# Performance work log

Hardware: AMD Instinct MI355X
Metric: run time of the kernel (lower is better)

Reference implementation:

```python
import jax, jax.numpy as jnp
import numpy as np

N_ATOMS = 50_000
N_PAIRS = 1_000_000
F_A = 75    # n_atom_input_feat
F_P = 14    # n_pair_input_feat
H = 50      # all hidden / output widths


def _glorot(key, shape):
    fan_in, fan_out = shape
    lim = np.sqrt(6.0 / (fan_in + fan_out)).astype(np.float32)
    return jax.random.uniform(key, shape, jnp.float32, -lim, lim)


def setup_inputs() -> dict:
    key = jax.random.key(0)
    ks = jax.random.split(key, 12)
    atom_features = jax.random.normal(ks[0], (N_ATOMS, F_A), jnp.float32)
    pair_features = jax.random.normal(ks[1], (N_PAIRS, F_P), jnp.float32)
    # per-pair anchor-atom segment id (sorted, as pairs are grouped by atom)
    pair_seg = jnp.sort(jax.random.randint(ks[2], (N_PAIRS,), 0, N_ATOMS, jnp.int32))
    atom_to_pair = jax.random.randint(ks[3], (N_PAIRS, 2), 0, N_ATOMS, jnp.int32)
    return {
        "atom_features": atom_features,
        "pair_features": pair_features,
        "pair_seg": pair_seg,
        "atom_to_pair": atom_to_pair,
        "W_AA": _glorot(ks[4], (F_A, H)), "b_AA": jnp.zeros((H,), jnp.float32),
        "W_PA": _glorot(ks[5], (F_P, H)), "b_PA": jnp.zeros((H,), jnp.float32),
        "W_A": _glorot(ks[6], (2 * H, H)), "b_A": jnp.zeros((H,), jnp.float32),
        "W_AP": _glorot(ks[7], (2 * F_A, H)), "b_AP": jnp.zeros((H,), jnp.float32),
        "W_PP": _glorot(ks[8], (F_P, H)), "b_PP": jnp.zeros((H,), jnp.float32),
        "W_P": _glorot(ks[9], (2 * H, H)), "b_P": jnp.zeros((H,), jnp.float32),
    }


def reference(atom_features, pair_features, pair_seg, atom_to_pair,
              W_AA, b_AA, W_PA, b_PA, W_A, b_A, W_AP, b_AP, W_PP, b_PP, W_P, b_P):
    act = jax.nn.relu
    n_atoms = atom_features.shape[0]
    n_pairs = pair_features.shape[0]

    # atom -> atom
    AA = act(atom_features @ W_AA + b_AA)                              # [Na, H]
    # pair -> atom: per-pair hidden, segment-summed to the anchor atom
    PA = act(pair_features @ W_PA + b_PA)                              # [Np, H]
    PA_sum = jax.ops.segment_sum(PA, pair_seg, num_segments=n_atoms)   # [Na, H]
    A = act(jnp.concatenate([AA, PA_sum], axis=1) @ W_A + b_A)         # [Na, H]

    # atom -> pair: gather both endpoints, (i,j) and (j,i) orderings
    ap = atom_features[atom_to_pair]                                   # [Np, 2, Fa]
    AP_ij = act(ap.reshape(n_pairs, 2 * ap.shape[-1]) @ W_AP + b_AP)
    AP_ji = act(ap[:, ::-1, :].reshape(n_pairs, 2 * ap.shape[-1]) @ W_AP + b_AP)
    # pair -> pair
    PP = act(pair_features @ W_PP + b_PP)
    P = act(jnp.concatenate([AP_ij + AP_ji, PP], axis=1) @ W_P + b_P)  # [Np, H]
    return A, P
```

## Files before the change

kernel.cpp:

```cpp
#include <hip/hip_runtime.h>
#include <hip/hip_bf16.h>

#define NA 50000
#define NP 1000000
#define FA 75
#define FP 14
#define H  50

typedef __attribute__((ext_vector_type(8))) short short8;
typedef __attribute__((ext_vector_type(4))) float f32x4;
typedef __attribute__((ext_vector_type(2))) float f32x2;

__device__ __forceinline__ ushort f2bf(float f) {
    union { float f; unsigned u; } v; v.f = f;
    unsigned r = v.u + 0x7FFF + ((v.u >> 16) & 1);
    return (ushort)(r >> 16);
}
__device__ __forceinline__ unsigned cvtpk(float lo, float hi) {
    unsigned r;
    asm("v_cvt_pk_bf16_f32 %0, %1, %2" : "=v"(r) : "v"(lo), "v"(hi));
    return r;
}
__device__ __forceinline__ ushort f2bf1(float f) { return (ushort)cvtpk(f, f); }
__device__ __forceinline__ unsigned pk_fp8(float u, float v) {
    unsigned r;
    asm("v_cvt_pk_fp8_f32 %0, %1, %2" : "=v"(r) : "v"(u), "v"(v));
    return r;
}
__device__ __forceinline__ float2 unpk_fp8(unsigned w) {
    float2 r;
    asm("v_cvt_pk_f32_fp8 %0, %1" : "=v"(r) : "v"(w));
    return r;
}
__device__ __forceinline__ short8 mk8(unsigned a, unsigned b, unsigned c, unsigned d) {
    union { unsigned u[4]; short8 s; } x; x.u[0]=a; x.u[1]=b; x.u[2]=c; x.u[3]=d; return x.s;
}

__global__ __launch_bounds__(256) void k_prep_frags(
    const float* __restrict__ W_P, const float* __restrict__ W_A,
    const float* __restrict__ W_PP, const float* __restrict__ W_PA,
    const float* __restrict__ W_AA, const float* __restrict__ W_AP,
    ushort* __restrict__ WPf, ushort* __restrict__ WAf, ushort* __restrict__ W2f,
    ushort* __restrict__ WPREf)
{
    const int t0 = blockIdx.x * 256 + threadIdx.x;
    const int STR = 16 * 256;
    for (int idx = t0; idx < 4*4*64*8; idx += STR) {
        int j = idx & 7, l = (idx >> 3) & 63, tn = (idx >> 9) & 3, tk = idx >> 11;
        int k = tk*32 + (l>>4)*8 + j;
        int c = tn*16 + (l&15);
        ushort vp = 0, va = 0;
        if (k < 100 && c < 50) { vp = f2bf(W_P[k*50+c]); va = f2bf(W_A[k*50+c]); }
        WPf[idx] = vp; WAf[idx] = va;
    }
    for (int idx = t0; idx < 8*64*8; idx += STR) {
        int j = idx & 7, l = (idx >> 3) & 63, tn = idx >> 9;
        int k = (l>>4)*8 + j;
        int c = (tn&3)*16 + (l&15);
        ushort v = 0;
        if (k < 14 && c < 50) v = f2bf(tn < 4 ? W_PP[k*50+c] : W_PA[k*50+c]);
        W2f[idx] = v;
    }
    for (int idx = t0; idx < 3*12*64*8; idx += STR) {
        int j = idx & 7, l = (idx >> 3) & 63;
        int g = idx >> 9;
        int tn = g % 12, tk = g / 12;
        int k = tk*32 + (l>>4)*8 + j;
        int sn = tn*16 + (l&15);
        int which = sn >> 6, col = sn & 63;
        ushort v = 0;
        if (k < FA && col < H) {
            float w = (which == 0) ? W_AA[k*H+col]
                    : (which == 1) ? W_AP[k*H+col]
                                   : W_AP[(FA+k)*H+col];
            v = f2bf(w);
        }
        WPREf[idx] = v;
    }
}

__global__ __launch_bounds__(256) void k_atom_pre(
    const float* __restrict__ af, const ushort* __restrict__ WPREf,
    const float* __restrict__ b_AA,
    ushort* __restrict__ AAb, ushort* __restrict__ UV8)
{
    __shared__ __align__(16) ushort sAF[64][104];
    const int t = threadIdx.x, lane = t & 63, w = t >> 6;
    const int a0 = blockIdx.x * 64, row0 = w * 16;

    for (int idx = t; idx < 64*96; idx += 256) {
        int r = idx / 96, c = idx % 96;
        int ag = a0 + r;
        float v = (c < FA && ag < NA) ? __builtin_nontemporal_load(&af[(size_t)ag*FA + c]) : 0.f;
        sAF[r][c] = f2bf(v);
    }
    __syncthreads();

    short8 afr[3];
    #pragma unroll
    for (int tk = 0; tk < 3; ++tk)
        afr[tk] = *(const short8*)&sAF[row0 + (lane&15)][tk*32 + (lane>>4)*8];

    const short8* B = (const short8*)WPREf;
    f32x4 acc[12];
    #pragma unroll
    for (int tn = 0; tn < 12; ++tn) acc[tn] = (f32x4){0.f, 0.f, 0.f, 0.f};
    #pragma unroll
    for (int tk = 0; tk < 3; ++tk) {
        #pragma unroll
        for (int tn = 0; tn < 12; ++tn) {
            short8 b = B[(tk*12 + tn)*64 + lane];
            acc[tn] = __builtin_amdgcn_mfma_f32_16x16x32_bf16(afr[tk], b, acc[tn], 0, 0, 0);
        }
    }

    #pragma unroll
    for (int tn = 0; tn < 4; ++tn) {
        int col = tn*16 + (lane&15);
        if (col < H) {
            float ba = b_AA[col];
            #pragma unroll
            for (int reg = 0; reg < 4; ++reg) {
                int atom = a0 + row0 + (lane>>4)*4 + reg;
                if (atom < NA) {
                    AAb[(size_t)atom*H + col] = f2bf(fmaxf(acc[tn][reg] + ba, 0.f));
                    UV8[(size_t)atom*64 + col] =
                        (ushort)pk_fp8(acc[4 + tn][reg], acc[8 + tn][reg]);
                }
            }
        }
    }
}

__global__ __launch_bounds__(256, 4) void k_pairs(
    const float* __restrict__ pf, const int* __restrict__ seg, const int* __restrict__ a2p,
    const ushort* __restrict__ UV8,
    const float* __restrict__ b_PP, const float* __restrict__ b_PA,
    const float* __restrict__ b_AP, const float* __restrict__ b_P,
    const ushort* __restrict__ WPf, const ushort* __restrict__ W2f,
    float* __restrict__ PAsum, float* __restrict__ Pout)
{
    __shared__ __align__(16) ushort sX[64][136];

    const int t = threadIdx.x;
    const int w = t >> 6, lane = t & 63;
    const int q = lane >> 4, m = lane & 15;
    const int p0 = blockIdx.x * 64;
    const int row0 = w * 16;
    const int p0w_u = __builtin_amdgcn_readfirstlane(p0 + row0);

    const int* a2ps = a2p + 2 * p0w_u;
    const int* segs = seg + p0w_u;
    int pi[16], pj[16], sg[16];
    #pragma unroll
    for (int it = 0; it < 16; ++it) {
        pi[it] = a2ps[2*it];
        pj[it] = a2ps[2*it + 1];
        sg[it] = segs[it];
    }

    const f32x2* pf2 = (const f32x2*)(pf + (size_t)(p0w_u + m) * FP);
    f32x2 g0 = {0.f,0.f}, g1 = {0.f,0.f}, g2 = {0.f,0.f}, g3 = {0.f,0.f};
    if (q == 0) {
        g0 = __builtin_nontemporal_load(&pf2[0]);
        g1 = __builtin_nontemporal_load(&pf2[1]);
        g2 = __builtin_nontemporal_load(&pf2[2]);
        g3 = __builtin_nontemporal_load(&pf2[3]);
    } else if (q == 1) {
        g0 = __builtin_nontemporal_load(&pf2[4]);
        g1 = __builtin_nontemporal_load(&pf2[5]);
        g2 = __builtin_nontemporal_load(&pf2[6]);
    }
    float bap = (lane < H) ? b_AP[lane] : 0.f;
    __builtin_amdgcn_sched_barrier(0);

    unsigned uvi[16], uvj[16];
    const unsigned lo2 = (unsigned)(lane << 1);
    #pragma unroll
    for (int it = 0; it < 8; ++it) {
        unsigned offi = ((unsigned)pi[it] << 7) | lo2;
        unsigned offj = ((unsigned)pj[it] << 7) | lo2;
        asm volatile("global_load_ushort %0, %1, %2"
                     : "=v"(uvi[it]) : "v"(offi), "s"(UV8));
        asm volatile("global_load_ushort %0, %1, %2"
                     : "=v"(uvj[it]) : "v"(offj), "s"(UV8));
    }
    #pragma unroll
    for (int it = 8; it < 16; ++it) {
        unsigned offi = ((unsigned)pi[it] << 7) | lo2;
        unsigned offj = ((unsigned)pj[it] << 7) | lo2;
        asm volatile("global_load_ushort %0, %1, %2"
                     : "=v"(uvi[it]) : "v"(offi), "s"(UV8));
        asm volatile("global_load_ushort %0, %1, %2"
                     : "=v"(uvj[it]) : "v"(offj), "s"(UV8));
    }

    if (lane < 16) {
        unsigned long long* rowp = (unsigned long long*)&sX[row0 + lane][100];
        #pragma unroll
        for (int d = 0; d < 7; ++d) rowp[d] = 0ull;
    }

    asm volatile("s_waitcnt vmcnt(16)" ::: "memory");
    __builtin_amdgcn_sched_barrier(0);
    #pragma unroll
    for (int it = 0; it < 8; ++it) {
        if (lane < H) {
            float2 fi = unpk_fp8(uvi[it]);
            float2 fj = unpk_fp8(uvj[it]);
            float aps = fmaxf(fi.x + fj.y + bap, 0.f) + fmaxf(fj.x + fi.y + bap, 0.f);
            sX[row0 + it][lane] = f2bf1(aps);
        }
    }
    asm volatile("s_waitcnt vmcnt(0)" ::: "memory");
    __builtin_amdgcn_sched_barrier(0);
    #pragma unroll
    for (int it = 8; it < 16; ++it) {
        if (lane < H) {
            float2 fi = unpk_fp8(uvi[it]);
            float2 fj = unpk_fp8(uvj[it]);
            float aps = fmaxf(fi.x + fj.y + bap, 0.f) + fmaxf(fj.x + fi.y + bap, 0.f);
            sX[row0 + it][lane] = f2bf1(aps);
        }
    }

    short8 afrag = mk8(cvtpk(g0.x, g0.y), cvtpk(g1.x, g1.y),
                       cvtpk(g2.x, g2.y), cvtpk(g3.x, g3.y));
    float pa[4][4];
    {
        const short8* B = (const short8*)W2f;
        #pragma unroll
        for (int tn = 0; tn < 8; ++tn) {
            f32x4 c = {0.f, 0.f, 0.f, 0.f};
            short8 b = B[tn*64 + lane];
            c = __builtin_amdgcn_mfma_f32_16x16x32_bf16(afrag, b, c, 0, 0, 0);
            int col = (tn&3)*16 + m;
            if (tn < 4) {
                if (col < H) {
                    float bias = b_PP[col];
                    #pragma unroll
                    for (int reg = 0; reg < 4; ++reg)
                        sX[row0 + q*4 + reg][H + col] = f2bf1(fmaxf(c[reg] + bias, 0.f));
                }
            } else {
                float bias = (col < H) ? b_PA[col] : 0.f;
                #pragma unroll
                for (int reg = 0; reg < 4; ++reg)
                    pa[tn-4][reg] = fmaxf(c[reg] + bias, 0.f);
            }
        }
    }

    #pragma unroll
    for (int tn4 = 0; tn4 < 4; ++tn4) {
        float v[16];
        #pragma unroll
        for (int g = 0; g < 4; ++g) {
            int src = m + (g << 4);
            #pragma unroll
            for (int r4 = 0; r4 < 4; ++r4)
                v[g*4 + r4] = __shfl(pa[tn4][r4], src, 64);
        }
        int col = tn4*16 + m;
        if (q == 0 && col < H) {
            float acc = v[0]; int cur = sg[0];
            #pragma unroll
            for (int r = 1; r < 16; ++r) {
                if (sg[r] != cur) {
                    atomicAdd(&PAsum[(size_t)cur*H + col], acc);
                    acc = 0.f; cur = sg[r];
                }
                acc += v[r];
            }
            atomicAdd(&PAsum[(size_t)cur*H + col], acc);
        }
    }

    asm volatile("s_waitcnt lgkmcnt(0)" ::: "memory");
    __builtin_amdgcn_sched_barrier(0);

    {
        short8 afr[4];
        #pragma unroll
        for (int tk = 0; tk < 4; ++tk)
            afr[tk] = *(const short8*)&sX[row0 + m][tk*32 + q*8];
        const short8* B = (const short8*)WPf;
        f32x4 acc[4];
        #pragma unroll
        for (int tn = 0; tn < 4; ++tn) acc[tn] = (f32x4){0.f, 0.f, 0.f, 0.f};
        #pragma unroll
        for (int tk = 0; tk < 4; ++tk) {
            #pragma unroll
            for (int tn = 0; tn < 4; ++tn) {
                short8 b = B[(tk*4 + tn)*64 + lane];
                acc[tn] = __builtin_amdgcn_mfma_f32_16x16x32_bf16(afr[tk], b, acc[tn], 0, 0, 0);
            }
        }
        #pragma unroll
        for (int tn = 0; tn < 4; ++tn) {
            int col = tn*16 + m;
            if (col < H) {
                float bp = b_P[col];
                #pragma unroll
                for (int reg = 0; reg < 4; ++reg) {
                    int row = row0 + q*4 + reg;
                    __builtin_nontemporal_store(fmaxf(acc[tn][reg] + bp, 0.f),
                                                &Pout[(size_t)(p0 + row)*H + col]);
                }
            }
        }
    }
}

__global__ __launch_bounds__(256) void k_A(
    const ushort* __restrict__ AAb, const float* __restrict__ PAsum,
    const ushort* __restrict__ WAf, const float* __restrict__ b_A,
    float* __restrict__ Aout)
{
    __shared__ __align__(16) ushort sX[64][136];
    const int t = threadIdx.x, lane = t & 63, w = t >> 6;
    const int a0 = blockIdx.x * 64;
    const int row0 = w * 16;

    for (int idx = t; idx < 64*50; idx += 256) {
        int r = idx / 50, c = idx % 50;
        int rg = a0 + r;
        ushort aa = 0; float ps = 0.f;
        if (rg < NA) {
            aa = __builtin_nontemporal_load(&AAb[(size_t)rg*H + c]);
            ps = __builtin_nontemporal_load(&PAsum[(size_t)rg*H + c]);
        }
        sX[r][c] = aa;
        sX[r][H + c] = f2bf1(ps);
    }
    for (int idx = t; idx < 64*28; idx += 256) {
        int r = idx / 28, c = 100 + idx % 28;
        sX[r][c] = 0;
    }
    __syncthreads();

    short8 afr[4];
    #pragma unroll
    for (int tk = 0; tk < 4; ++tk)
        afr[tk] = *(const short8*)&sX[row0 + (lane&15)][tk*32 + (lane>>4)*8];
    const short8* B = (const short8*)WAf;
    f32x4 acc[4];
    #pragma unroll
    for (int tn = 0; tn < 4; ++tn) acc[tn] = (f32x4){0.f, 0.f, 0.f, 0.f};
    #pragma unroll
    for (int tk = 0; tk < 4; ++tk) {
        #pragma unroll
        for (int tn = 0; tn < 4; ++tn) {
            short8 b = B[(tk*4 + tn)*64 + lane];
            acc[tn] = __builtin_amdgcn_mfma_f32_16x16x32_bf16(afr[tk], b, acc[tn], 0, 0, 0);
        }
    }
    #pragma unroll
    for (int tn = 0; tn < 4; ++tn) {
        int col = tn*16 + (lane&15);
        if (col < H) {
            float ba = b_A[col];
            #pragma unroll
            for (int reg = 0; reg < 4; ++reg) {
                int row = row0 + (lane>>4)*4 + reg;
                int rg = a0 + row;
                if (rg < NA)
                    __builtin_nontemporal_store(fmaxf(acc[tn][reg] + ba, 0.f),
                                                &Aout[(size_t)rg*H + col]);
            }
        }
    }
}

extern "C" void kernel_launch(void* const* d_in, const int* in_sizes, int n_in,
                              void* d_out, int out_size, void* d_ws, size_t ws_size,
                              hipStream_t stream)
{
    const float* af   = (const float*)d_in[0];
    const float* pf   = (const float*)d_in[1];
    const int*   seg  = (const int*)d_in[2];
    const int*   a2p  = (const int*)d_in[3];
    const float* W_AA = (const float*)d_in[4];
    const float* b_AA = (const float*)d_in[5];
    const float* W_PA = (const float*)d_in[6];
    const float* b_PA = (const float*)d_in[7];
    const float* W_A  = (const float*)d_in[8];
    const float* b_A  = (const float*)d_in[9];
    const float* W_AP = (const float*)d_in[10];
    const float* b_AP = (const float*)d_in[11];
    const float* W_PP = (const float*)d_in[12];
    const float* b_PP = (const float*)d_in[13];
    const float* W_P  = (const float*)d_in[14];
    const float* b_P  = (const float*)d_in[15];

    float* Aout = (float*)d_out;
    float* Pout = (float*)d_out + (size_t)NA * H;

    ushort*   AAb   = (ushort*)d_ws;
    float*    PAsum = (float*)(AAb + (size_t)NA * H);
    ushort*   UV8   = (ushort*)(PAsum + (size_t)NA * H);
    ushort*   WPf   = UV8 + (size_t)NA * 64;
    ushort*   WAf   = WPf + 4*4*64*8;
    ushort*   W2f   = WAf + 4*4*64*8;
    ushort*   WPREf = W2f + 8*64*8;

    hipMemsetAsync(PAsum, 0, (size_t)NA * H * sizeof(float), stream);
    k_prep_frags<<<16, 256, 0, stream>>>(W_P, W_A, W_PP, W_PA, W_AA, W_AP,
                                         WPf, WAf, W2f, WPREf);
    k_atom_pre<<<(NA + 63) / 64, 256, 0, stream>>>(af, WPREf, b_AA, AAb, UV8);
    k_pairs<<<NP / 64, 256, 0, stream>>>(pf, seg, a2p, UV8, b_PP, b_PA, b_AP, b_P,
                                         WPf, W2f, PAsum, Pout);
    k_A<<<(NA + 63) / 64, 256, 0, stream>>>(AAb, PAsum, WAf, b_A, Aout);
}
```

Baseline: 254.7 us.

## Process two 16-pair tiles per wave and use regular stores for outputs

Each wave now loops over two consecutive 16-pair tiles, so each block covers 128 pairs and the grid is halved. The two-phase split wait on the gather loads is collapsed into a single wait per tile, and the nontemporal output stores for P and A become plain stores. The goal is to amortize per-block setup such as bias loads and LDS padding zeroing, and to let the cache handle the output writes. The risks are less memory-level parallelism from the serialized tiles and the lost early overlap of the gather loads with the first half of the compute.

```diff
diff --git a/kernel.cpp b/kernel.cpp
--- a/kernel.cpp
+++ b/kernel.cpp
@@ -145,55 +145,11 @@
     const int t = threadIdx.x;
     const int w = t >> 6, lane = t & 63;
     const int q = lane >> 4, m = lane & 15;
-    const int p0 = blockIdx.x * 64;
     const int row0 = w * 16;
-    const int p0w_u = __builtin_amdgcn_readfirstlane(p0 + row0);
-
-    const int* a2ps = a2p + 2 * p0w_u;
-    const int* segs = seg + p0w_u;
-    int pi[16], pj[16], sg[16];
-    #pragma unroll
-    for (int it = 0; it < 16; ++it) {
-        pi[it] = a2ps[2*it];
-        pj[it] = a2ps[2*it + 1];
-        sg[it] = segs[it];
-    }
-
-    const f32x2* pf2 = (const f32x2*)(pf + (size_t)(p0w_u + m) * FP);
-    f32x2 g0 = {0.f,0.f}, g1 = {0.f,0.f}, g2 = {0.f,0.f}, g3 = {0.f,0.f};
-    if (q == 0) {
-        g0 = __builtin_nontemporal_load(&pf2[0]);
-        g1 = __builtin_nontemporal_load(&pf2[1]);
-        g2 = __builtin_nontemporal_load(&pf2[2]);
-        g3 = __builtin_nontemporal_load(&pf2[3]);
-    } else if (q == 1) {
-        g0 = __builtin_nontemporal_load(&pf2[4]);
-        g1 = __builtin_nontemporal_load(&pf2[5]);
-        g2 = __builtin_nontemporal_load(&pf2[6]);
-    }
+    const int base = blockIdx.x * 128 + w * 32;
+    if (base >= NP) return;
+
     float bap = (lane < H) ? b_AP[lane] : 0.f;
-    __builtin_amdgcn_sched_barrier(0);
-
-    unsigned uvi[16], uvj[16];
-    const unsigned lo2 = (unsigned)(lane << 1);
-    #pragma unroll
-    for (int it = 0; it < 8; ++it) {
-        unsigned offi = ((unsigned)pi[it] << 7) | lo2;
-        unsigned offj = ((unsigned)pj[it] << 7) | lo2;
-        asm volatile("global_load_ushort %0, %1, %2"
-                     : "=v"(uvi[it]) : "v"(offi), "s"(UV8));
-        asm volatile("global_load_ushort %0, %1, %2"
-                     : "=v"(uvj[it]) : "v"(offj), "s"(UV8));
-    }
-    #pragma unroll
-    for (int it = 8; it < 16; ++it) {
-        unsigned offi = ((unsigned)pi[it] << 7) | lo2;
-        unsigned offj = ((unsigned)pj[it] << 7) | lo2;
-        asm volatile("global_load_ushort %0, %1, %2"
-                     : "=v"(uvi[it]) : "v"(offi), "s"(UV8));
-        asm volatile("global_load_ushort %0, %1, %2"
-                     : "=v"(uvj[it]) : "v"(offj), "s"(UV8));
-    }
 
     if (lane < 16) {
         unsigned long long* rowp = (unsigned long long*)&sX[row0 + lane][100];
@@ -201,114 +157,146 @@
         for (int d = 0; d < 7; ++d) rowp[d] = 0ull;
     }
 
-    asm volatile("s_waitcnt vmcnt(16)" ::: "memory");
-    __builtin_amdgcn_sched_barrier(0);
-    #pragma unroll
-    for (int it = 0; it < 8; ++it) {
-        if (lane < H) {
-            float2 fi = unpk_fp8(uvi[it]);
-            float2 fj = unpk_fp8(uvj[it]);
-            float aps = fmaxf(fi.x + fj.y + bap, 0.f) + fmaxf(fj.x + fi.y + bap, 0.f);
-            sX[row0 + it][lane] = f2bf1(aps);
-        }
-    }
-    asm volatile("s_waitcnt vmcnt(0)" ::: "memory");
-    __builtin_amdgcn_sched_barrier(0);
-    #pragma unroll
-    for (int it = 8; it < 16; ++it) {
-        if (lane < H) {
-            float2 fi = unpk_fp8(uvi[it]);
-            float2 fj = unpk_fp8(uvj[it]);
-            float aps = fmaxf(fi.x + fj.y + bap, 0.f) + fmaxf(fj.x + fi.y + bap, 0.f);
-            sX[row0 + it][lane] = f2bf1(aps);
-        }
-    }
-
-    short8 afrag = mk8(cvtpk(g0.x, g0.y), cvtpk(g1.x, g1.y),
-                       cvtpk(g2.x, g2.y), cvtpk(g3.x, g3.y));
-    float pa[4][4];
-    {
-        const short8* B = (const short8*)W2f;
-        #pragma unroll
-        for (int tn = 0; tn < 8; ++tn) {
-            f32x4 c = {0.f, 0.f, 0.f, 0.f};
-            short8 b = B[tn*64 + lane];
-            c = __builtin_amdgcn_mfma_f32_16x16x32_bf16(afrag, b, c, 0, 0, 0);
-            int col = (tn&3)*16 + m;
-            if (tn < 4) {
-                if (col < H) {
-                    float bias = b_PP[col];
+    for (int s = 0; s < 2; ++s) {
+        const int p0w_u = __builtin_amdgcn_readfirstlane(base + s * 16);
+
+        const int* a2ps = a2p + 2 * p0w_u;
+        const int* segs = seg + p0w_u;
+        int pi[16], pj[16], sg[16];
+        #pragma unroll
+        for (int it = 0; it < 16; ++it) {
+            pi[it] = a2ps[2*it];
+            pj[it] = a2ps[2*it + 1];
+            sg[it] = segs[it];
+        }
+
+        const f32x2* pf2 = (const f32x2*)(pf + (size_t)(p0w_u + m) * FP);
+        f32x2 g0 = {0.f,0.f}, g1 = {0.f,0.f}, g2 = {0.f,0.f}, g3 = {0.f,0.f};
+        if (q == 0) {
+            g0 = __builtin_nontemporal_load(&pf2[0]);
+            g1 = __builtin_nontemporal_load(&pf2[1]);
+            g2 = __builtin_nontemporal_load(&pf2[2]);
+            g3 = __builtin_nontemporal_load(&pf2[3]);
+        } else if (q == 1) {
+            g0 = __builtin_nontemporal_load(&pf2[4]);
+            g1 = __builtin_nontemporal_load(&pf2[5]);
+            g2 = __builtin_nontemporal_load(&pf2[6]);
+        }
+        __builtin_amdgcn_sched_barrier(0);
+
+        unsigned uvi[16], uvj[16];
+        const unsigned lo2 = (unsigned)(lane << 1);
+        #pragma unroll
+        for (int it = 0; it < 16; ++it) {
+            unsigned offi = ((unsigned)pi[it] << 7) | lo2;
+            unsigned offj = ((unsigned)pj[it] << 7) | lo2;
+            asm volatile("global_load_ushort %0, %1, %2"
+                         : "=v"(uvi[it]) : "v"(offi), "s"(UV8));
+            asm volatile("global_load_ushort %0, %1, %2"
+                         : "=v"(uvj[it]) : "v"(offj), "s"(UV8));
+        }
+
+        asm volatile("s_waitcnt vmcnt(0)" ::: "memory");
+        __builtin_amdgcn_sched_barrier(0);
+
+        #pragma unroll
+        for (int it = 0; it < 16; ++it) {
+            if (lane < H) {
+                float2 fi = unpk_fp8(uvi[it]);
+                float2 fj = unpk_fp8(uvj[it]);
+                float aps = fmaxf(fi.x + fj.y + bap, 0.f) + fmaxf(fj.x + fi.y + bap, 0.f);
+                sX[row0 + it][lane] = f2bf1(aps);
+            }
+        }
+
+        short8 afrag = mk8(cvtpk(g0.x, g0.y), cvtpk(g1.x, g1.y),
+                           cvtpk(g2.x, g2.y), cvtpk(g3.x, g3.y));
+        float pa[4][4];
+        {
+            const short8* B = (const short8*)W2f;
+            #pragma unroll
+            for (int tn = 0; tn < 8; ++tn) {
+                f32x4 c = {0.f, 0.f, 0.f, 0.f};
+                short8 b = B[tn*64 + lane];
+                c = __builtin_amdgcn_mfma_f32_16x16x32_bf16(afrag, b, c, 0, 0, 0);
+                int col = (tn&3)*16 + m;
+                if (tn < 4) {
+                    if (col < H) {
+                        float bias = b_PP[col];
+                        #pragma unroll
+                        for (int reg = 0; reg < 4; ++reg)
+                            sX[row0 + q*4 + reg][H + col] = f2bf1(fmaxf(c[reg] + bias, 0.f));
+                    }
+                } else {
+                    float bias = (col < H) ? b_PA[col] : 0.f;
                     #pragma unroll
                     for (int reg = 0; reg < 4; ++reg)
-                        sX[row0 + q*4 + reg][H + col] = f2bf1(fmaxf(c[reg] + bias, 0.f));
+                        pa[tn-4][reg] = fmaxf(c[reg] + bias, 0.f);
                 }
-            } else {
-                float bias = (col < H) ? b_PA[col] : 0.f;
+            }
+        }
+
+        #pragma unroll
+        for (int tn4 = 0; tn4 < 4; ++tn4) {
+            float v[16];
+            #pragma unroll
+            for (int g = 0; g < 4; ++g) {
+                int src = m + (g << 4);
                 #pragma unroll
-                for (int reg = 0; reg < 4; ++reg)
-                    pa[tn-4][reg] = fmaxf(c[reg] + bias, 0.f);
-            }
-        }
-    }
-
-    #pragma unroll
-    for (int tn4 = 0; tn4 < 4; ++tn4) {
-        float v[16];
-        #pragma unroll
-        for (int g = 0; g < 4; ++g) {
-            int src = m + (g << 4);
-            #pragma unroll
-            for (int r4 = 0; r4 < 4; ++r4)
-                v[g*4 + r4] = __shfl(pa[tn4][r4], src, 64);
-        }
-        int col = tn4*16 + m;
-        if (q == 0 && col < H) {
-            float acc = v[0]; int cur = sg[0];
-            #pragma unroll
-            for (int r = 1; r < 16; ++r) {
-                if (sg[r] != cur) {
-                    atomicAdd(&PAsum[(size_t)cur*H + col], acc);
-                    acc = 0.f; cur = sg[r];
+                for (int r4 = 0; r4 < 4; ++r4)
+                    v[g*4 + r4] = __shfl(pa[tn4][r4], src, 64);
+            }
+            int col = tn4*16 + m;
+            if (q == 0 && col < H) {
+                float acc = v[0]; int cur = sg[0];
+                #pragma unroll
+                for (int r = 1; r < 16; ++r) {
+                    if (sg[r] != cur) {
+                        atomicAdd(&PAsum[(size_t)cur*H + col], acc);
+                        acc = 0.f; cur = sg[r];
+                    }
+                    acc += v[r];
                 }
-                acc += v[r];
-            }
-            atomicAdd(&PAsum[(size_t)cur*H + col], acc);
-        }
-    }
-
-    asm volatile("s_waitcnt lgkmcnt(0)" ::: "memory");
-    __builtin_amdgcn_sched_barrier(0);
-
-    {
-        short8 afr[4];
-        #pragma unroll
-        for (int tk = 0; tk < 4; ++tk)
-            afr[tk] = *(const short8*)&sX[row0 + m][tk*32 + q*8];
-        const short8* B = (const short8*)WPf;
-        f32x4 acc[4];
-        #pragma unroll
-        for (int tn = 0; tn < 4; ++tn) acc[tn] = (f32x4){0.f, 0.f, 0.f, 0.f};
-        #pragma unroll
-        for (int tk = 0; tk < 4; ++tk) {
+                atomicAdd(&PAsum[(size_t)cur*H + col], acc);
+            }
+        }
+
+        asm volatile("s_waitcnt lgkmcnt(0)" ::: "memory");
+        __builtin_amdgcn_sched_barrier(0);
+
+        {
+            short8 afr[4];
+            #pragma unroll
+            for (int tk = 0; tk < 4; ++tk)
+                afr[tk] = *(const short8*)&sX[row0 + m][tk*32 + q*8];
+            const short8* B = (const short8*)WPf;
+            f32x4 acc[4];
+            #pragma unroll
+            for (int tn = 0; tn < 4; ++tn) acc[tn] = (f32x4){0.f, 0.f, 0.f, 0.f};
+            #pragma unroll
+            for (int tk = 0; tk < 4; ++tk) {
+                #pragma unroll
+                for (int tn = 0; tn < 4; ++tn) {
+                    short8 b = B[(tk*4 + tn)*64 + lane];
+                    acc[tn] = __builtin_amdgcn_mfma_f32_16x16x32_bf16(afr[tk], b, acc[tn], 0, 0, 0);
+                }
+            }
             #pragma unroll
             for (int tn = 0; tn < 4; ++tn) {
-                short8 b = B[(tk*4 + tn)*64 + lane];
-                acc[tn] = __builtin_amdgcn_mfma_f32_16x16x32_bf16(afr[tk], b, acc[tn], 0, 0, 0);
-            }
-        }
-        #pragma unroll
-        for (int tn = 0; tn < 4; ++tn) {
-            int col = tn*16 + m;
-            if (col < H) {
-                float bp = b_P[col];
-                #pragma unroll
-                for (int reg = 0; reg < 4; ++reg) {
-                    int row = row0 + q*4 + reg;
-                    __builtin_nontemporal_store(fmaxf(acc[tn][reg] + bp, 0.f),
-                                                &Pout[(size_t)(p0 + row)*H + col]);
+                int col = tn*16 + m;
+                if (col < H) {
+                    float bp = b_P[col];
+                    #pragma unroll
+                    for (int reg = 0; reg < 4; ++reg) {
+                        int row = q*4 + reg;
+                        Pout[(size_t)(p0w_u + row)*H + col] = fmaxf(acc[tn][reg] + bp, 0.f);
+                    }
                 }
             }
         }
+
+        asm volatile("s_waitcnt lgkmcnt(0)" ::: "memory");
+        __builtin_amdgcn_sched_barrier(0);
     }
 }
 
@@ -364,9 +352,7 @@
             for (int reg = 0; reg < 4; ++reg) {
                 int row = row0 + (lane>>4)*4 + reg;
                 int rg = a0 + row;
-                if (rg < NA)
-                    __builtin_nontemporal_store(fmaxf(acc[tn][reg] + ba, 0.f),
-                                                &Aout[(size_t)rg*H + col]);
+                if (rg < NA) Aout[(size_t)rg*H + col] = fmaxf(acc[tn][reg] + ba, 0.f);
             }
         }
     }
@@ -408,7 +394,8 @@
     k_prep_frags<<<16, 256, 0, stream>>>(W_P, W_A, W_PP, W_PA, W_AA, W_AP,
                                          WPf, WAf, W2f, WPREf);
     k_atom_pre<<<(NA + 63) / 64, 256, 0, stream>>>(af, WPREf, b_AA, AAb, UV8);
-    k_pairs<<<NP / 64, 256, 0, stream>>>(pf, seg, a2p, UV8, b_PP, b_PA, b_AP, b_P,
-                                         WPf, W2f, PAsum, Pout);
+    k_pairs<<<(NP + 127) / 128, 256, 0, stream>>>(pf, seg, a2p, UV8,
+                                                  b_PP, b_PA, b_AP, b_P,
+                                                  WPf, W2f, PAsum, Pout);
     k_A<<<(NA + 63) / 64, 256, 0, stream>>>(AAb, PAsum, WAf, b_A, Aout);
 }
```

New measurement: 225.5 us. 1.13x faster.
